# Performance work log

Measured on AMD Instinct MI355X. Metric: run time of the kernel, lower is better.

## Reference

```python
import jax, jax.numpy as jnp
import numpy as np

H, HD, C = 16, 64, 64            # num_heads, head_dim, mini_batch_size
BASE_LR = 1.0
EPS = 1e-6                        # ttt LN eps (ln_fwd / ln_fused_l2_bwd)


def _l2norm(x):
    return x / jnp.maximum(jnp.linalg.norm(x, axis=-1, keepdims=True), 1e-12)


def _ln_fwd(x, g, b):
    mu = x.mean(-1, keepdims=True)
    var = x.var(-1, keepdims=True)
    return g * ((x - mu) * jax.lax.rsqrt(var + EPS)) + b


def _ln_l2_bwd(x, tgt, g, b):
    # gradient of ||LN(x)*g+b - tgt||^2 / 2 wrt x
    D = x.shape[-1]
    mu = x.mean(-1, keepdims=True)
    var = x.var(-1, keepdims=True)
    std = jnp.sqrt(var + EPS)
    xh = (x - mu) / std
    gout = (g * xh + b) - tgt
    gxh = gout * g
    return (D * gxh - gxh.sum(-1, keepdims=True) - xh * (gxh * xh).sum(-1, keepdims=True)) / (D * std)


def setup_inputs() -> dict:
    key = jax.random.key(0)
    ks = jax.random.split(key, 12)
    B, L, D = 4, 8192, 1024
    std = 0.02
    return {
        'hidden_states': jax.random.normal(ks[0], (B, L, D), jnp.float32),
        'wq_w': jax.random.normal(ks[1], (D, D), jnp.float32) * std,
        'wq_b': jnp.zeros((D,), jnp.float32),
        'wk_w': jax.random.normal(ks[2], (D, D), jnp.float32) * std,
        'wk_b': jnp.zeros((D,), jnp.float32),
        'wv_w': jax.random.normal(ks[3], (D, D), jnp.float32) * std,
        'wv_b': jnp.zeros((D,), jnp.float32),
        'wo_w': jax.random.normal(ks[4], (D, D), jnp.float32) * std,
        'wo_b': jnp.zeros((D,), jnp.float32),
        'ttt_norm_weight': jnp.ones((H, HD), jnp.float32),
        'ttt_norm_bias': jnp.zeros((H, HD), jnp.float32),
        'ttt_lr_weight': jax.random.normal(ks[5], (H, 1, D), jnp.float32) * std,
        'ttt_lr_bias': jnp.zeros((H, 1), jnp.float32),
        'W1': jax.random.normal(ks[6], (H, HD, HD), jnp.float32) * std,
        'b1': jnp.zeros((H, 1, HD), jnp.float32),
        'post_norm_w': jnp.ones((D,), jnp.float32),
        'post_norm_b': jnp.zeros((D,), jnp.float32),
    }


def _forward(hidden_states, wq_w, wq_b, wk_w, wk_b, wv_w, wv_b, wo_w, wo_b,
             ttt_norm_weight, ttt_norm_bias, ttt_lr_weight, ttt_lr_bias,
             W1, b1, post_norm_w, post_norm_b):
    B, L, D = hidden_states.shape
    NC = L // C
    XQ = (hidden_states @ wq_w.T + wq_b).reshape(B, L, H, HD)
    XK = (hidden_states @ wk_w.T + wk_b).reshape(B, L, H, HD)
    XV = (hidden_states @ wv_w.T + wv_b).reshape(B, L, H, HD)
    XQ = _l2norm(XQ)
    XK = _l2norm(XK)
    # ln_reconstruction_target (uses sample std, ddof=1, eps=1e-5 on std)
    d = XV - XK
    mu = d.mean(-1, keepdims=True)
    sd = d.std(-1, keepdims=True, ddof=1)
    XV = ttt_norm_weight[None, None] * ((d - mu) / (sd + 1e-5)) + ttt_norm_bias[None, None] + XK
    # reshape to mini-batches: [B,H,NC,C,HD]
    Xmb = hidden_states.reshape(B, NC, C, D)
    to_mb = lambda t: t.transpose(0, 2, 1, 3).reshape(B, H, NC, C, HD)
    XQ, XK, XV = to_mb(XQ), to_mb(XK), to_mb(XV)
    # eta: sigmoid lr gate per token, row-broadcast over mini-batch
    ttt_lr = jax.nn.sigmoid(jnp.einsum('bnkc,hdc->bhnkd', Xmb, ttt_lr_weight)
                            + ttt_lr_bias.reshape(1, H, 1, 1, 1))     # [B,H,NC,C,1]
    eta = jnp.swapaxes(ttt_lr, -1, -2) * (BASE_LR / HD / C)           # [B,H,NC,1,C]
    mask = jnp.tril(jnp.ones((C, C), hidden_states.dtype))
    g = ttt_norm_weight[None, :, None, :]
    bta = ttt_norm_bias[None, :, None, :]
    W0 = jnp.broadcast_to(W1[None], (B, H, HD, HD))
    b0 = jnp.broadcast_to(b1[None], (B, H, 1, HD))

    def step(carry, xs):
        W, bvec = carry
        xq, xk, xv, eta_row = xs                      # eta_row: [B,H,1,C]
        Z1 = xk @ W + bvec                            # [B,H,C,HD]
        grad = _ln_l2_bwd(Z1, xv - xk, g, bta)        # [B,H,C,HD]
        Attn = mask * jnp.einsum('bhid,bhjd->bhij', xq, xk)   # [B,H,C,C]
        eta_full = jnp.broadcast_to(eta_row, Attn.shape)      # [B,H,C,C]
        b1_bar = bvec - (mask * eta_full) @ grad              # [B,H,C,HD]
        Z1_bar = xq @ W - (eta_full * Attn) @ grad + b1_bar
        last_eta = eta_full[..., -1, :, None]                 # [B,H,C,1]
        W_new = W - jnp.einsum('bhcd,bhce->bhde', last_eta * xk, grad)
        b_new = bvec - (last_eta * grad).sum(-2, keepdims=True)
        out = xq + _ln_fwd(Z1_bar, g, bta)
        return (W_new, b_new), out

    xs = (jnp.moveaxis(XQ, 2, 0), jnp.moveaxis(XK, 2, 0),
          jnp.moveaxis(XV, 2, 0), jnp.moveaxis(eta, 2, 0))
    _, outs = jax.lax.scan(step, (W0, b0), xs)        # outs: [NC,B,H,C,HD]
    y = jnp.moveaxis(outs, 0, 2).reshape(B, H, L, HD).transpose(0, 2, 1, 3).reshape(B, L, D)
    # post LayerNorm (eps=1e-6) + output projection
    mu2 = y.mean(-1, keepdims=True)
    var2 = y.var(-1, keepdims=True)
    y = post_norm_w * ((y - mu2) * jax.lax.rsqrt(var2 + 1e-6)) + post_norm_b
    return y @ wo_w.T + wo_b


def reference(hidden_states, wq_w, wq_b, wk_w, wk_b, wv_w, wv_b, wo_w, wo_b,
              ttt_norm_weight, ttt_norm_bias, ttt_lr_weight, ttt_lr_bias,
              W1, b1, post_norm_w, post_norm_b):
    return _forward(hidden_states, wq_w, wq_b, wk_w, wk_b, wv_w, wv_b, wo_w, wo_b,
                    ttt_norm_weight, ttt_norm_bias, ttt_lr_weight, ttt_lr_bias,
                    W1, b1, post_norm_w, post_norm_b)
```

## Files before the change

kernel.cpp:

```cpp
#include <hip/hip_runtime.h>


typedef __attribute__((ext_vector_type(8))) short short8;
typedef __attribute__((ext_vector_type(4))) float f32x4;
typedef __attribute__((ext_vector_type(4))) unsigned short us4;

__device__ __forceinline__ float bf2f(unsigned short s) {
  union { unsigned int u; float f; } c;
  c.u = ((unsigned int)s) << 16;
  return c.f;
}
__device__ __forceinline__ unsigned short f2bf(float f) {
  union { float f; unsigned int u; } c;
  c.f = f;
  unsigned int u = c.u;
  return (unsigned short)((u + 0x7FFFu + ((u >> 16) & 1u)) >> 16);
}

__device__ __forceinline__ void gload_lds16(const void* g, void* l) {
  __builtin_amdgcn_global_load_lds(
      (const __attribute__((address_space(1))) unsigned int*)g,
      (__attribute__((address_space(3))) unsigned int*)l, 16, 0, 0);
}

__device__ __forceinline__ float dpp16_sum(float x) {
  int v = __float_as_int(x);
  x += __int_as_float(__builtin_amdgcn_update_dpp(v, v, 0xB1, 0xF, 0xF, true));
  v = __float_as_int(x);
  x += __int_as_float(__builtin_amdgcn_update_dpp(v, v, 0x4E, 0xF, 0xF, true));
  v = __float_as_int(x);
  x += __int_as_float(__builtin_amdgcn_update_dpp(v, v, 0x141, 0xF, 0xF, true));
  v = __float_as_int(x);
  x += __int_as_float(__builtin_amdgcn_update_dpp(v, v, 0x140, 0xF, 0xF, true));
  return x;
}

__device__ __forceinline__ void barrier_fast() {
  __builtin_amdgcn_sched_barrier(0);
  asm volatile("s_waitcnt lgkmcnt(0)" ::: "memory");
  __builtin_amdgcn_s_barrier();
  asm volatile("" ::: "memory");
  __builtin_amdgcn_sched_barrier(0);
}
__device__ __forceinline__ void bar_nowait() {
  __builtin_amdgcn_sched_barrier(0);
  asm volatile("" ::: "memory");
  __builtin_amdgcn_s_barrier();
  asm volatile("" ::: "memory");
  __builtin_amdgcn_sched_barrier(0);
}

__global__ __launch_bounds__(256) void cvt_f32_bf16(
    const float* __restrict__ in, unsigned short* __restrict__ out, long n) {
  long i = ((long)blockIdx.x * 256 + threadIdx.x) * 4;
  if (i + 3 < n) {
    float4 v = *(const float4*)&in[i];
    us4 o = { f2bf(v.x), f2bf(v.y), f2bf(v.z), f2bf(v.w) };
    *(us4*)&out[i] = o;
  }
}

__global__ __launch_bounds__(256) void build_wcat(
    const float* __restrict__ wq, const float* __restrict__ wk,
    const float* __restrict__ wv, const float* __restrict__ lrw,
    const float* __restrict__ wqb, const float* __restrict__ wkb,
    const float* __restrict__ wvb, const float* __restrict__ lrb,
    unsigned short* __restrict__ Wcat, float* __restrict__ biasc) {
  int i = blockIdx.x * 256 + threadIdx.x;
  int row = i >> 10, col = i & 1023;
  float v;
  if (row < 1024)      v = wq[i];
  else if (row < 2048) v = wk[i - 1048576];
  else if (row < 3072) v = wv[i - 2097152];
  else if (row < 3088) v = lrw[(row - 3072) * 1024 + col];
  else                 v = 0.f;
  Wcat[i] = f2bf(v);
  if (i < 3328) {
    float bv;
    if (i < 1024)      bv = wqb[i];
    else if (i < 2048) bv = wkb[i - 1024];
    else if (i < 3072) bv = wvb[i - 2048];
    else if (i < 3088) bv = lrb[i - 3072];
    else               bv = 0.f;
    biasc[i] = bv;
  }
}

template <int WRITE_BF16>
__global__ __launch_bounds__(512, 1) void gemm256(
    const unsigned short* __restrict__ A, const unsigned short* __restrict__ B,
    const float* __restrict__ bias, void* __restrict__ Cout,
    long M, long N, long K, int NTILN, long ldc) {
  __shared__ __align__(16) unsigned short g_lds[65536];
  char* ldsc = (char*)g_lds;
  const int tid = threadIdx.x, lane = tid & 63, wid = tid >> 6;
  const int wm = wid >> 2, wn = wid & 3;
  const int l15 = lane & 15, lg = lane >> 4;

  unsigned nwg = gridDim.x, bid = blockIdx.x;
  unsigned cpx = nwg >> 3;
  unsigned swz = (bid & 7) * cpx + (bid >> 3);
  unsigned nidx = swz % (unsigned)NTILN, midx = swz / (unsigned)NTILN;
  const long m0 = (long)midx * 256, n0 = (long)nidx * 256;
  const long ldab = K * 2;

  const int srow = wid * 16 + (lane >> 2);
  const int scol = ((lane & 3) * 16) ^ (((lane >> 3) & 3) << 4);
  const int sdst = wid * 1024;
  const char* Ab = (const char*)A;
  const char* Bb = (const char*)B;

  const int acol = (lg * 16) ^ (((l15 >> 1) & 3) << 4);
  const int aro = (wm * 128 + l15) * 64 + acol;
  const int bro = 65536 + (wn * 64 + l15) * 64 + acol;

#define STG_A(tt, h, bb)                                                     \
  gload_lds16(Ab + (size_t)(m0 + (h) * 128 + srow) * ldab + (size_t)(tt) * 64 \
                  + scol,                                                     \
              ldsc + (bb) * 16384 + (h) * 8192 + sdst)
#define STG_B(tt, h, bb)                                                     \
  gload_lds16(Bb + (size_t)(n0 + (h) * 128 + srow) * ldab + (size_t)(tt) * 64 \
                  + scol,                                                     \
              ldsc + 65536 + (bb) * 16384 + (h) * 8192 + sdst)

  f32x4 acc[8][4];
#pragma unroll
  for (int m = 0; m < 8; ++m)
#pragma unroll
    for (int n = 0; n < 4; ++n) acc[m][n] = (f32x4){0.f, 0.f, 0.f, 0.f};

  const int NT = (int)(K >> 5);

#pragma unroll
  for (int tt = 0; tt < 3; ++tt) {
    STG_A(tt, 0, tt); STG_A(tt, 1, tt);
    STG_B(tt, 0, tt); STG_B(tt, 1, tt);
  }
  asm volatile("s_waitcnt vmcnt(8)" ::: "memory");
  bar_nowait();

#pragma unroll 1
  for (int t = 0; t < NT; ++t) {
    const int buf = t & 3, sb = (t + 3) & 3;
    const bool doStage = (t + 3 < NT);
    const char* ab = ldsc + buf * 16384 + aro;
    const char* bb = ldsc + buf * 16384 + bro;

    short8 av[4], bv[4];
#pragma unroll
    for (int i = 0; i < 4; ++i) av[i] = *(const short8*)(ab + i * 1024);
#pragma unroll
    for (int nf = 0; nf < 4; ++nf) bv[nf] = *(const short8*)(bb + nf * 1024);
    if (doStage) { STG_A(t + 3, 0, sb); STG_A(t + 3, 1, sb); }
    bar_nowait();
    __builtin_amdgcn_s_setprio(1);
#pragma unroll
    for (int i = 0; i < 4; ++i)
#pragma unroll
      for (int nf = 0; nf < 4; ++nf)
        acc[i][nf] = __builtin_amdgcn_mfma_f32_16x16x32_bf16(av[i], bv[nf],
                                                             acc[i][nf], 0, 0, 0);
    __builtin_amdgcn_s_setprio(0);
    bar_nowait();

#pragma unroll
    for (int i = 0; i < 4; ++i) av[i] = *(const short8*)(ab + 4096 + i * 1024);
    if (doStage) { STG_B(t + 3, 0, sb); STG_B(t + 3, 1, sb); }
    bar_nowait();
    __builtin_amdgcn_s_setprio(1);
#pragma unroll
    for (int i = 0; i < 4; ++i)
#pragma unroll
      for (int nf = 0; nf < 4; ++nf)
        acc[4 + i][nf] = __builtin_amdgcn_mfma_f32_16x16x32_bf16(
            av[i], bv[nf], acc[4 + i][nf], 0, 0, 0);
    __builtin_amdgcn_s_setprio(0);
    asm volatile("s_waitcnt vmcnt(8)" ::: "memory");
    bar_nowait();
  }
#undef STG_A
#undef STG_B

#pragma unroll
  for (int mf = 0; mf < 8; ++mf) {
    long r0 = m0 + wm * 128 + mf * 16 + lg * 4;
#pragma unroll
    for (int nf = 0; nf < 4; ++nf) {
      long c = n0 + wn * 64 + nf * 16 + l15;
      float bvv = bias ? bias[c] : 0.f;
#pragma unroll
      for (int j = 0; j < 4; ++j) {
        float v = acc[mf][nf][j] + bvv;
        if (WRITE_BF16)
          ((unsigned short*)Cout)[(r0 + j) * ldc + c] = f2bf(v);
        else
          ((float*)Cout)[(r0 + j) * ldc + c] = v;
      }
    }
  }
}

__global__ __launch_bounds__(256) void stage2(
    const unsigned short* __restrict__ QKVL, const float* __restrict__ tnw,
    const float* __restrict__ tnb, unsigned short* __restrict__ XQn,
    unsigned short* __restrict__ XKn, unsigned short* __restrict__ TGT,
    float* __restrict__ eta_buf) {
  int wid = threadIdx.x >> 6, lane = threadIdx.x & 63;
  long idx = (long)blockIdx.x * 4 + wid;
  long t = idx >> 4;
  int h = (int)(idx & 15);
  size_t base = (size_t)t * 3328;
  float q = bf2f(QKVL[base + h * 64 + lane]);
  float k = bf2f(QKVL[base + 1024 + h * 64 + lane]);
  float v = bf2f(QKVL[base + 2048 + h * 64 + lane]);
  float sq = q * q, sk = k * k;
#pragma unroll
  for (int o = 1; o < 64; o <<= 1) {
    sq += __shfl_xor(sq, o);
    sk += __shfl_xor(sk, o);
  }
  float qn = q / fmaxf(sqrtf(sq), 1e-12f);
  float kn = k / fmaxf(sqrtf(sk), 1e-12f);
  float d = v - kn;
  float s1 = d, s2 = d * d;
#pragma unroll
  for (int o = 1; o < 64; o <<= 1) {
    s1 += __shfl_xor(s1, o);
    s2 += __shfl_xor(s2, o);
  }
  float mu = s1 * 0.015625f;
  float var1 = fmaxf(s2 - 64.f * mu * mu, 0.f) * (1.f / 63.f);
  float sd = sqrtf(var1);
  float tgt = tnw[h * 64 + lane] * ((d - mu) / (sd + 1e-5f)) + tnb[h * 64 + lane];
  size_t ob = (size_t)t * 1024 + h * 64 + lane;
  XQn[ob] = f2bf(qn);
  XKn[ob] = f2bf(kn);
  TGT[ob] = f2bf(tgt);
  if (lane == 0) {
    float logit = bf2f(QKVL[base + 3072 + h]);
    float sig = 1.f / (1.f + expf(-logit));
    long bb = t >> 13, l = t & 8191;
    eta_buf[(size_t)(bb * 16 + h) * 8192 + l] = sig * (1.f / 4096.f);
  }
}

__global__ __launch_bounds__(512, 1) void ttt_scan(
    const unsigned short* __restrict__ XQ, const unsigned short* __restrict__ XK,
    const unsigned short* __restrict__ TG, const float* __restrict__ eta_buf,
    const float* __restrict__ W1, const float* __restrict__ b1,
    const float* __restrict__ tnw, const float* __restrict__ tnb,
    float* __restrict__ y) {
  const int bh = blockIdx.x;
  const int b = bh >> 4, h = bh & 15;
  const int tid = threadIdx.x;
  const int lane = tid & 63, wid = tid >> 6;
  const bool isA = wid < 4;
  const int q = wid & 3;
  const int l15 = lane & 15, lg = lane >> 4;

  __shared__ __align__(16) unsigned short xq_s[2][64 * 72];
  __shared__ __align__(16) unsigned short tg_s[2][64 * 72];
  __shared__ __align__(16) unsigned short xk_s[2][64 * 72];
  __shared__ __align__(16) unsigned short gc_s[64 * 72];
  __shared__ __align__(16) unsigned short gradT[64 * 72];
  __shared__ __align__(16) unsigned short xkTe[64 * 72];
  __shared__ __align__(16) unsigned short WT_b[2][64 * 72];
  __shared__ float eta_s[2][64];
  __shared__ float bpart[4][64];

  const size_t tokb = (size_t)b * 8192;
  const int col0 = h * 64;
  const int rr_ = q * 16 + (lane >> 3);
  const int c8_ = (lane & 7) * 8;

  short8 pA0[2], pA1[2], pB0[2];
  float peta = 0.f;
  float bstv[4], gwv[4], gbv[4];
  f32x4 Wreg[4];

  if (isA) {
#pragma unroll
    for (int n = 0; n < 4; ++n) {
      int e = n * 16 + l15;
      bstv[n] = b1[h * 64 + e];
      gwv[n] = tnw[h * 64 + e];
      gbv[n] = tnb[h * 64 + e];
    }
#pragma unroll
    for (int j = 0; j < 2; ++j) {
      size_t g = (tokb + rr_ + j * 8) * 1024 + col0 + c8_;
      pA0[j] = *(const short8*)&XQ[g];
      pA1[j] = *(const short8*)&TG[g];
    }
#pragma unroll
    for (int j = 0; j < 2; ++j) {
      int rr = rr_ + j * 8;
      *(short8*)&xq_s[0][rr * 72 + c8_] = pA0[j];
      *(short8*)&tg_s[0][rr * 72 + c8_] = pA1[j];
    }
#pragma unroll
    for (int j = 0; j < 2; ++j) {
      size_t g = (tokb + 64 + rr_ + j * 8) * 1024 + col0 + c8_;
      pA0[j] = *(const short8*)&XQ[g];
      pA1[j] = *(const short8*)&TG[g];
    }
  } else {
#pragma unroll
    for (int j = 0; j < 2; ++j)
      pB0[j] = *(const short8*)&XK[(tokb + rr_ + j * 8) * 1024 + col0 + c8_];
#pragma unroll
    for (int j = 0; j < 2; ++j)
      *(short8*)&xk_s[0][(rr_ + j * 8) * 72 + c8_] = pB0[j];
#pragma unroll
    for (int j = 0; j < 2; ++j)
      pB0[j] = *(const short8*)&XK[(tokb + 64 + rr_ + j * 8) * 1024 + col0 + c8_];
#pragma unroll
    for (int n = 0; n < 4; ++n)
#pragma unroll
      for (int jj = 0; jj < 4; ++jj) {
        int d = q * 16 + lg * 4 + jj, e = n * 16 + l15;
        float w = W1[h * 4096 + d * 64 + e];
        Wreg[n][jj] = w;
        WT_b[0][e * 72 + d] = f2bf(w);
      }
    if (wid == 4) {
      eta_s[0][lane] = eta_buf[(size_t)bh * 8192 + lane];
      peta = eta_buf[(size_t)bh * 8192 + 64 + lane];
    }
  }
  __syncthreads();

  for (int nc = 0; nc < 128; ++nc) {
    const int p = nc & 1;
    const unsigned short* WTc = WT_b[p];
    unsigned short* WTn = WT_b[p ^ 1];

    if (isA) {
      if (nc) {
#pragma unroll
        for (int n = 0; n < 4; ++n) {
          int e = n * 16 + l15;
          bstv[n] -= bpart[0][e] + bpart[1][e] + bpart[2][e] + bpart[3][e];
        }
      }
      if (nc + 1 < 128) {
#pragma unroll
        for (int j = 0; j < 2; ++j) {
          int rr = rr_ + j * 8;
          *(short8*)&xq_s[p ^ 1][rr * 72 + c8_] = pA0[j];
          *(short8*)&tg_s[p ^ 1][rr * 72 + c8_] = pA1[j];
        }
      }
      if (nc + 2 < 128) {
#pragma unroll
        for (int j = 0; j < 2; ++j) {
          size_t g = (tokb + (nc + 2) * 64 + rr_ + j * 8) * 1024 + col0 + c8_;
          pA0[j] = *(const short8*)&XQ[g];
          pA1[j] = *(const short8*)&TG[g];
        }
      }
      f32x4 accZ[4];
#pragma unroll
      for (int n = 0; n < 4; ++n)
        accZ[n] = (f32x4){bstv[n], bstv[n], bstv[n], bstv[n]};
      __builtin_amdgcn_s_setprio(1);
#pragma unroll
      for (int kk = 0; kk < 2; ++kk) {
        const int ko = kk * 32 + lg * 8;
        short8 a_xk = *(const short8*)&xk_s[p][(q * 16 + l15) * 72 + ko];
#pragma unroll
        for (int n = 0; n < 4; ++n) {
          short8 b_w = *(const short8*)&WTc[(n * 16 + l15) * 72 + ko];
          accZ[n] = __builtin_amdgcn_mfma_f32_16x16x32_bf16(a_xk, b_w, accZ[n], 0, 0, 0);
        }
      }
      __builtin_amdgcn_s_setprio(0);
      float grv[4][4];
#pragma unroll
      for (int j = 0; j < 4; ++j) {
        const int r = q * 16 + lg * 4 + j;
        float z[4], s1 = 0.f, s2 = 0.f;
#pragma unroll
        for (int n = 0; n < 4; ++n) {
          z[n] = accZ[n][j];
          s1 += z[n];
          s2 += z[n] * z[n];
        }
        s1 = dpp16_sum(s1);
        s2 = dpp16_sum(s2);
        float mu = s1 * 0.015625f;
        float var = s2 * 0.015625f - mu * mu;
        float rstd = rsqrtf(var + 1e-6f);
        float xh[4], gx[4], s3 = 0.f, s4 = 0.f;
#pragma unroll
        for (int n = 0; n < 4; ++n) {
          xh[n] = (z[n] - mu) * rstd;
          float tg = bf2f(tg_s[p][r * 72 + n * 16 + l15]);
          float go = gwv[n] * xh[n] + gbv[n] - tg;
          gx[n] = go * gwv[n];
          s3 += gx[n];
          s4 += gx[n] * xh[n];
        }
        s3 = dpp16_sum(s3);
        s4 = dpp16_sum(s4);
#pragma unroll
        for (int n = 0; n < 4; ++n)
          grv[n][j] = (64.f * gx[n] - s3 - xh[n] * s4) * rstd * 0.015625f;
      }
#pragma unroll
      for (int n = 0; n < 4; ++n) {
        us4 pk = {f2bf(grv[n][0]), f2bf(grv[n][1]), f2bf(grv[n][2]),
                  f2bf(grv[n][3])};
        *(us4*)&gradT[(n * 16 + l15) * 72 + q * 16 + lg * 4] = pk;
      }
    } else {
      if (nc + 1 < 128) {
#pragma unroll
        for (int j = 0; j < 2; ++j)
          *(short8*)&xk_s[p ^ 1][(rr_ + j * 8) * 72 + c8_] = pB0[j];
        if (wid == 4) eta_s[p ^ 1][lane] = peta;
      }
      if (nc + 2 < 128) {
#pragma unroll
        for (int j = 0; j < 2; ++j)
          pB0[j] = *(const short8*)
              &XK[(tokb + (nc + 2) * 64 + rr_ + j * 8) * 1024 + col0 + c8_];
        if (wid == 4) peta = eta_buf[(size_t)bh * 8192 + (nc + 2) * 64 + lane];
      }
#pragma unroll
      for (int it = 0; it < 4; ++it) {
        int c0 = q * 16 + it * 4;
        us4 pk;
#pragma unroll
        for (int u = 0; u < 4; ++u)
          pk[u] = f2bf(-eta_s[p][c0 + u] * bf2f(xk_s[p][(c0 + u) * 72 + lane]));
        *(us4*)&xkTe[lane * 72 + c0] = pk;
      }
      f32x4 accA[4];
#pragma unroll
      for (int n = 0; n < 4; ++n) accA[n] = (f32x4){0.f, 0.f, 0.f, 0.f};
      __builtin_amdgcn_s_setprio(1);
#pragma unroll
      for (int kk = 0; kk < 2; ++kk) {
        const int ko = kk * 32 + lg * 8;
        short8 a_xq = *(const short8*)&xq_s[p][(q * 16 + l15) * 72 + ko];
#pragma unroll
        for (int n = 0; n < 4; ++n) {
          short8 b_k = *(const short8*)&xk_s[p][(n * 16 + l15) * 72 + ko];
          accA[n] = __builtin_amdgcn_mfma_f32_16x16x32_bf16(a_xq, b_k, accA[n], 0, 0, 0);
        }
      }
      __builtin_amdgcn_s_setprio(0);
#pragma unroll
      for (int j = 0; j < 4; ++j) {
        const int r = q * 16 + lg * 4 + j;
#pragma unroll
        for (int n = 0; n < 4; ++n) {
          int cj = n * 16 + l15;
          float v = (cj <= r) ? (-eta_s[p][cj] * (1.f + accA[n][j])) : 0.f;
          gc_s[r * 72 + cj] = f2bf(v);
        }
      }
    }
    barrier_fast();

    if (isA) {
      f32x4 accZb[4];
#pragma unroll
      for (int n = 0; n < 4; ++n)
        accZb[n] = (f32x4){bstv[n], bstv[n], bstv[n], bstv[n]};
      __builtin_amdgcn_s_setprio(1);
#pragma unroll
      for (int kk = 0; kk < 2; ++kk) {
        const int ko = kk * 32 + lg * 8;
        short8 a_xq = *(const short8*)&xq_s[p][(q * 16 + l15) * 72 + ko];
        short8 a_gc = *(const short8*)&gc_s[(q * 16 + l15) * 72 + ko];
#pragma unroll
        for (int n = 0; n < 4; ++n) {
          short8 b_w = *(const short8*)&WTc[(n * 16 + l15) * 72 + ko];
          short8 b_g = *(const short8*)&gradT[(n * 16 + l15) * 72 + ko];
          accZb[n] = __builtin_amdgcn_mfma_f32_16x16x32_bf16(a_xq, b_w, accZb[n], 0, 0, 0);
          accZb[n] = __builtin_amdgcn_mfma_f32_16x16x32_bf16(a_gc, b_g, accZb[n], 0, 0, 0);
        }
      }
      __builtin_amdgcn_s_setprio(0);
#pragma unroll
      for (int j = 0; j < 4; ++j) {
        const int r = q * 16 + lg * 4 + j;
        float z[4], s1 = 0.f, s2 = 0.f;
#pragma unroll
        for (int n = 0; n < 4; ++n) {
          z[n] = accZb[n][j];
          s1 += z[n];
          s2 += z[n] * z[n];
        }
        s1 = dpp16_sum(s1);
        s2 = dpp16_sum(s2);
        float mu = s1 * 0.015625f;
        float var = s2 * 0.015625f - mu * mu;
        float rstd = rsqrtf(var + 1e-6f);
        size_t gbase = (tokb + nc * 64 + r) * 1024 + col0;
#pragma unroll
        for (int n = 0; n < 4; ++n) {
          int e = n * 16 + l15;
          float ov = bf2f(xq_s[p][r * 72 + e]) + gwv[n] * ((z[n] - mu) * rstd) + gbv[n];
          y[gbase + e] = ov;
        }
      }
    } else {
      f32x4 accW[4];
#pragma unroll
      for (int n = 0; n < 4; ++n) accW[n] = Wreg[n];
      __builtin_amdgcn_s_setprio(1);
#pragma unroll
      for (int kk = 0; kk < 2; ++kk) {
        const int ko = kk * 32 + lg * 8;
        short8 a_ke = *(const short8*)&xkTe[(q * 16 + l15) * 72 + ko];
#pragma unroll
        for (int n = 0; n < 4; ++n) {
          short8 b_g = *(const short8*)&gradT[(n * 16 + l15) * 72 + ko];
          accW[n] = __builtin_amdgcn_mfma_f32_16x16x32_bf16(a_ke, b_g, accW[n], 0, 0, 0);
        }
      }
      __builtin_amdgcn_s_setprio(0);
#pragma unroll
      for (int n = 0; n < 4; ++n) {
        Wreg[n] = accW[n];
        us4 pk = {f2bf(accW[n][0]), f2bf(accW[n][1]), f2bf(accW[n][2]),
                  f2bf(accW[n][3])};
        *(us4*)&WTn[(n * 16 + l15) * 72 + q * 16 + lg * 4] = pk;
      }
      {
        float s = 0.f;
#pragma unroll
        for (int it = 0; it < 4; ++it) {
          us4 gv = *(const us4*)&gradT[lane * 72 + q * 16 + it * 4];
#pragma unroll
          for (int u = 0; u < 4; ++u)
            s += eta_s[p][q * 16 + it * 4 + u] * bf2f(gv[u]);
        }
        bpart[q][lane] = s;
      }
    }
    barrier_fast();
  }
}

__global__ __launch_bounds__(256) void postnorm(
    const float* __restrict__ yv, const float* __restrict__ pw,
    const float* __restrict__ pb, unsigned short* __restrict__ yn) {
  int t = blockIdx.x;
  int tid = threadIdx.x, lane = tid & 63, wid = tid >> 6;
  const float* row = yv + (size_t)t * 1024;
  float4 v = *(const float4*)&row[tid * 4];
  float s1 = v.x + v.y + v.z + v.w;
  float s2 = v.x * v.x + v.y * v.y + v.z * v.z + v.w * v.w;
#pragma unroll
  for (int o = 1; o < 64; o <<= 1) {
    s1 += __shfl_xor(s1, o);
    s2 += __shfl_xor(s2, o);
  }
  __shared__ float r1[4], r2[4];
  if (lane == 0) {
    r1[wid] = s1;
    r2[wid] = s2;
  }
  __syncthreads();
  s1 = r1[0] + r1[1] + r1[2] + r1[3];
  s2 = r2[0] + r2[1] + r2[2] + r2[3];
  float mu = s1 * (1.f / 1024.f);
  float var = s2 * (1.f / 1024.f) - mu * mu;
  float rstd = rsqrtf(var + 1e-6f);
  int c = tid * 4;
  us4 o4 = {f2bf(pw[c] * ((v.x - mu) * rstd) + pb[c]),
            f2bf(pw[c + 1] * ((v.y - mu) * rstd) + pb[c + 1]),
            f2bf(pw[c + 2] * ((v.z - mu) * rstd) + pb[c + 2]),
            f2bf(pw[c + 3] * ((v.w - mu) * rstd) + pb[c + 3])};
  *(us4*)&yn[(size_t)t * 1024 + c] = o4;
}

extern "C" void kernel_launch(void* const* d_in, const int* in_sizes, int n_in,
                              void* d_out, int out_size, void* d_ws,
                              size_t ws_size, hipStream_t stream) {
  const float* hs  = (const float*)d_in[0];
  const float* wqw = (const float*)d_in[1];
  const float* wqb = (const float*)d_in[2];
  const float* wkw = (const float*)d_in[3];
  const float* wkb = (const float*)d_in[4];
  const float* wvw = (const float*)d_in[5];
  const float* wvb = (const float*)d_in[6];
  const float* wow = (const float*)d_in[7];
  const float* wob = (const float*)d_in[8];
  const float* tnw = (const float*)d_in[9];
  const float* tnb = (const float*)d_in[10];
  const float* lrw = (const float*)d_in[11];
  const float* lrb = (const float*)d_in[12];
  const float* W1  = (const float*)d_in[13];
  const float* b1  = (const float*)d_in[14];
  const float* pnw = (const float*)d_in[15];
  const float* pnb = (const float*)d_in[16];

  const size_t OFF_WCAT  = 67108864;
  const size_t OFF_BIASC = OFF_WCAT + 6815744;
  const size_t OFF_WOBF  = OFF_BIASC + 16384;
  const size_t OFF_QKVL  = OFF_WOBF + 2097152;
  const size_t OFF_XK    = OFF_QKVL + 218103808;
  const size_t OFF_TGT   = OFF_XK + 67108864;
  const size_t OFF_ETA   = OFF_TGT + 67108864;
  const size_t NEEDED    = OFF_ETA + 2097152;
  if (ws_size < NEEDED) return;

  char* ws = (char*)d_ws;
  unsigned short* hs_bf = (unsigned short*)ws;
  unsigned short* XQn   = (unsigned short*)ws;
  unsigned short* Wcat  = (unsigned short*)(ws + OFF_WCAT);
  float* biasc          = (float*)(ws + OFF_BIASC);
  unsigned short* wo_bf = (unsigned short*)(ws + OFF_WOBF);
  unsigned short* QKVL  = (unsigned short*)(ws + OFF_QKVL);
  float* yv             = (float*)(ws + OFF_QKVL);
  unsigned short* ynorm = (unsigned short*)(ws + OFF_QKVL + 134217728);
  unsigned short* XKn   = (unsigned short*)(ws + OFF_XK);
  unsigned short* TGT   = (unsigned short*)(ws + OFF_TGT);
  float* eta_buf        = (float*)(ws + OFF_ETA);

  cvt_f32_bf16<<<32768, 256, 0, stream>>>(hs, hs_bf, 33554432L);
  build_wcat<<<13312, 256, 0, stream>>>(wqw, wkw, wvw, lrw, wqb, wkb, wvb, lrb,
                                        Wcat, biasc);
  cvt_f32_bf16<<<1024, 256, 0, stream>>>(wow, wo_bf, 1048576L);
  gemm256<1><<<1664, 512, 0, stream>>>(hs_bf, Wcat, biasc, QKVL,
                                       32768L, 3328L, 1024L, 13, 3328L);
  stage2<<<131072, 256, 0, stream>>>(QKVL, tnw, tnb, XQn, XKn, TGT, eta_buf);
  ttt_scan<<<64, 512, 0, stream>>>(XQn, XKn, TGT, eta_buf, W1, b1, tnw, tnb, yv);
  postnorm<<<32768, 256, 0, stream>>>(yv, pnw, pnb, ynorm);
  gemm256<0><<<512, 512, 0, stream>>>(ynorm, wo_bf, wob, d_out,
                                      32768L, 1024L, 1024L, 4, 1024L);
}
```

Baseline: 956.2 us.

## Fuse QKV projection with L2-norm, target LN and eta into GEMM epilogue

Reorders the concatenated QKV weight so each 256-column GEMM tile holds one head's q, k, v and lr-logit columns. The per-head L2 normalisation, reconstruction-target LayerNorm and sigmoid eta are then computed in the GEMM epilogue, and the separate stage2 kernel is removed. This avoids writing and re-reading the large bf16 QKVL intermediate, at the cost of padding N from 3328 to 4096, which adds GEMM work. It also hoists the LDS loads ahead of the MFMAs in the W update of the scan kernel and reshuffles the workspace layout.

```diff
diff --git a/kernel.cpp b/kernel.cpp
--- a/kernel.cpp
+++ b/kernel.cpp
@@ -68,21 +68,211 @@
     unsigned short* __restrict__ Wcat, float* __restrict__ biasc) {
   int i = blockIdx.x * 256 + threadIdx.x;
   int row = i >> 10, col = i & 1023;
+  int h = row >> 8, o = row & 255;
   float v;
-  if (row < 1024)      v = wq[i];
-  else if (row < 2048) v = wk[i - 1048576];
-  else if (row < 3072) v = wv[i - 2097152];
-  else if (row < 3088) v = lrw[(row - 3072) * 1024 + col];
-  else                 v = 0.f;
+  if (o < 64)        v = wq[(h * 64 + o) * 1024 + col];
+  else if (o < 128)  v = wk[(h * 64 + o - 64) * 1024 + col];
+  else if (o < 192)  v = wv[(h * 64 + o - 128) * 1024 + col];
+  else if (o == 192) v = lrw[h * 1024 + col];
+  else               v = 0.f;
   Wcat[i] = f2bf(v);
-  if (i < 3328) {
+  if (i < 4096) {
+    int hh = i >> 8, oo = i & 255;
     float bv;
-    if (i < 1024)      bv = wqb[i];
-    else if (i < 2048) bv = wkb[i - 1024];
-    else if (i < 3072) bv = wvb[i - 2048];
-    else if (i < 3088) bv = lrb[i - 3072];
-    else               bv = 0.f;
+    if (oo < 64)        bv = wqb[hh * 64 + oo];
+    else if (oo < 128)  bv = wkb[hh * 64 + oo - 64];
+    else if (oo < 192)  bv = wvb[hh * 64 + oo - 128];
+    else if (oo == 192) bv = lrb[hh];
+    else                bv = 0.f;
     biasc[i] = bv;
+  }
+}
+
+__global__ __launch_bounds__(512, 1) void gemm256_qkv(
+    const unsigned short* __restrict__ A, const unsigned short* __restrict__ B,
+    const float* __restrict__ bias, const float* __restrict__ tnw,
+    const float* __restrict__ tnb, unsigned short* __restrict__ XQn,
+    unsigned short* __restrict__ XKn, unsigned short* __restrict__ TGT,
+    float* __restrict__ eta, long M, long K) {
+  __shared__ __align__(16) unsigned short g_lds[65536];
+  char* ldsc = (char*)g_lds;
+  const int tid = threadIdx.x, lane = tid & 63, wid = tid >> 6;
+  const int wm = wid >> 2, wn = wid & 3;
+  const int l15 = lane & 15, lg = lane >> 4;
+  const int NTILN = 16;
+
+  unsigned nwg = gridDim.x, bid = blockIdx.x;
+  unsigned cpx = nwg >> 3;
+  unsigned swz = (bid & 7) * cpx + (bid >> 3);
+  unsigned nidx = swz % (unsigned)NTILN, midx = swz / (unsigned)NTILN;
+  const long m0 = (long)midx * 256, n0 = (long)nidx * 256;
+  const long ldab = K * 2;
+
+  const int srow = wid * 16 + (lane >> 2);
+  const int scol = ((lane & 3) * 16) ^ (((lane >> 3) & 3) << 4);
+  const int sdst = wid * 1024;
+  const char* Ab = (const char*)A;
+  const char* Bb = (const char*)B;
+
+  const int acol = (lg * 16) ^ (((l15 >> 1) & 3) << 4);
+  const int aro = (wm * 128 + l15) * 64 + acol;
+  const int bro = 65536 + (wn * 64 + l15) * 64 + acol;
+
+#define STG_A(tt, h, bb)                                                      \
+  gload_lds16(Ab + (size_t)(m0 + (h) * 128 + srow) * ldab + (size_t)(tt) * 64 \
+                  + scol,                                                     \
+              ldsc + (bb) * 16384 + (h) * 8192 + sdst)
+#define STG_B(tt, h, bb)                                                      \
+  gload_lds16(Bb + (size_t)(n0 + (h) * 128 + srow) * ldab + (size_t)(tt) * 64 \
+                  + scol,                                                     \
+              ldsc + 65536 + (bb) * 16384 + (h) * 8192 + sdst)
+
+  f32x4 acc[8][4];
+#pragma unroll
+  for (int m = 0; m < 8; ++m)
+#pragma unroll
+    for (int n = 0; n < 4; ++n) acc[m][n] = (f32x4){0.f, 0.f, 0.f, 0.f};
+
+  const int NT = (int)(K >> 5);
+
+#pragma unroll
+  for (int tt = 0; tt < 3; ++tt) {
+    STG_A(tt, 0, tt); STG_A(tt, 1, tt);
+    STG_B(tt, 0, tt); STG_B(tt, 1, tt);
+  }
+  asm volatile("s_waitcnt vmcnt(8)" ::: "memory");
+  bar_nowait();
+
+#pragma unroll 1
+  for (int t = 0; t < NT; ++t) {
+    const int buf = t & 3, sb = (t + 3) & 3;
+    const bool doStage = (t + 3 < NT);
+    const char* ab = ldsc + buf * 16384 + aro;
+    const char* bb = ldsc + buf * 16384 + bro;
+
+    short8 av[4], bv[4];
+#pragma unroll
+    for (int i = 0; i < 4; ++i) av[i] = *(const short8*)(ab + i * 1024);
+#pragma unroll
+    for (int nf = 0; nf < 4; ++nf) bv[nf] = *(const short8*)(bb + nf * 1024);
+    if (doStage) { STG_A(t + 3, 0, sb); STG_A(t + 3, 1, sb); }
+    bar_nowait();
+    __builtin_amdgcn_s_setprio(1);
+#pragma unroll
+    for (int i = 0; i < 4; ++i)
+#pragma unroll
+      for (int nf = 0; nf < 4; ++nf)
+        acc[i][nf] = __builtin_amdgcn_mfma_f32_16x16x32_bf16(av[i], bv[nf],
+                                                             acc[i][nf], 0, 0, 0);
+    __builtin_amdgcn_s_setprio(0);
+    bar_nowait();
+
+#pragma unroll
+    for (int i = 0; i < 4; ++i) av[i] = *(const short8*)(ab + 4096 + i * 1024);
+    if (doStage) { STG_B(t + 3, 0, sb); STG_B(t + 3, 1, sb); }
+    bar_nowait();
+    __builtin_amdgcn_s_setprio(1);
+#pragma unroll
+    for (int i = 0; i < 4; ++i)
+#pragma unroll
+      for (int nf = 0; nf < 4; ++nf)
+        acc[4 + i][nf] = __builtin_amdgcn_mfma_f32_16x16x32_bf16(
+            av[i], bv[nf], acc[4 + i][nf], 0, 0, 0);
+    __builtin_amdgcn_s_setprio(0);
+    asm volatile("s_waitcnt vmcnt(8)" ::: "memory");
+    bar_nowait();
+  }
+#undef STG_A
+#undef STG_B
+
+  const int h = (int)nidx;
+  float bcol[4], twv[4], tbv[4];
+#pragma unroll
+  for (int nf = 0; nf < 4; ++nf) {
+    bcol[nf] = bias[n0 + wn * 64 + nf * 16 + l15];
+    twv[nf] = tnw[h * 64 + nf * 16 + l15];
+    tbv[nf] = tnb[h * 64 + nf * 16 + l15];
+  }
+  __syncthreads();
+  unsigned short* kn_s = g_lds;
+
+  if (wn == 0) {
+#pragma unroll
+    for (int mf = 0; mf < 8; ++mf)
+#pragma unroll
+      for (int j = 0; j < 4; ++j) {
+        float v[4], s2 = 0.f;
+#pragma unroll
+        for (int nf = 0; nf < 4; ++nf) {
+          v[nf] = acc[mf][nf][j] + bcol[nf];
+          s2 += v[nf] * v[nf];
+        }
+        s2 = dpp16_sum(s2);
+        float rn = 1.f / fmaxf(sqrtf(s2), 1e-12f);
+        size_t tt = (size_t)(m0 + wm * 128 + mf * 16 + lg * 4 + j);
+#pragma unroll
+        for (int nf = 0; nf < 4; ++nf)
+          XQn[tt * 1024 + h * 64 + nf * 16 + l15] = f2bf(v[nf] * rn);
+      }
+  } else if (wn == 1) {
+#pragma unroll
+    for (int mf = 0; mf < 8; ++mf)
+#pragma unroll
+      for (int j = 0; j < 4; ++j) {
+        float v[4], s2 = 0.f;
+#pragma unroll
+        for (int nf = 0; nf < 4; ++nf) {
+          v[nf] = acc[mf][nf][j] + bcol[nf];
+          s2 += v[nf] * v[nf];
+        }
+        s2 = dpp16_sum(s2);
+        float rn = 1.f / fmaxf(sqrtf(s2), 1e-12f);
+        size_t tt = (size_t)(m0 + wm * 128 + mf * 16 + lg * 4 + j);
+        int lr_ = wm * 128 + mf * 16 + lg * 4 + j;
+#pragma unroll
+        for (int nf = 0; nf < 4; ++nf) {
+          unsigned short kb = f2bf(v[nf] * rn);
+          XKn[tt * 1024 + h * 64 + nf * 16 + l15] = kb;
+          kn_s[lr_ * 72 + nf * 16 + l15] = kb;
+        }
+      }
+  }
+  __syncthreads();
+  if (wn == 2) {
+#pragma unroll
+    for (int mf = 0; mf < 8; ++mf)
+#pragma unroll
+      for (int j = 0; j < 4; ++j) {
+        int lr_ = wm * 128 + mf * 16 + lg * 4 + j;
+        float dv[4], s1 = 0.f, s2 = 0.f;
+#pragma unroll
+        for (int nf = 0; nf < 4; ++nf) {
+          float kn = bf2f(kn_s[lr_ * 72 + nf * 16 + l15]);
+          dv[nf] = acc[mf][nf][j] + bcol[nf] - kn;
+          s1 += dv[nf];
+          s2 += dv[nf] * dv[nf];
+        }
+        s1 = dpp16_sum(s1);
+        s2 = dpp16_sum(s2);
+        float mu = s1 * 0.015625f;
+        float var1 = fmaxf(s2 - 64.f * mu * mu, 0.f) * (1.f / 63.f);
+        float rs = 1.f / (sqrtf(var1) + 1e-5f);
+        size_t tt = (size_t)(m0 + wm * 128 + mf * 16 + lg * 4 + j);
+#pragma unroll
+        for (int nf = 0; nf < 4; ++nf)
+          TGT[tt * 1024 + h * 64 + nf * 16 + l15] =
+              f2bf(twv[nf] * ((dv[nf] - mu) * rs) + tbv[nf]);
+      }
+  } else if (wn == 3 && l15 == 0) {
+#pragma unroll
+    for (int mf = 0; mf < 8; ++mf)
+#pragma unroll
+      for (int j = 0; j < 4; ++j) {
+        size_t tt = (size_t)(m0 + wm * 128 + mf * 16 + lg * 4 + j);
+        float lgt = acc[mf][0][j] + bcol[0];
+        float sig = 1.f / (1.f + expf(-lgt));
+        eta[((tt >> 13) * 16 + h) * 8192 + (tt & 8191)] = sig * (1.f / 4096.f);
+      }
   }
 }
 
@@ -114,11 +304,11 @@
   const int aro = (wm * 128 + l15) * 64 + acol;
   const int bro = 65536 + (wn * 64 + l15) * 64 + acol;
 
-#define STG_A(tt, h, bb)                                                     \
+#define STG_A(tt, h, bb)                                                      \
   gload_lds16(Ab + (size_t)(m0 + (h) * 128 + srow) * ldab + (size_t)(tt) * 64 \
                   + scol,                                                     \
               ldsc + (bb) * 16384 + (h) * 8192 + sdst)
-#define STG_B(tt, h, bb)                                                     \
+#define STG_B(tt, h, bb)                                                      \
   gload_lds16(Bb + (size_t)(n0 + (h) * 128 + srow) * ldab + (size_t)(tt) * 64 \
                   + scol,                                                     \
               ldsc + 65536 + (bb) * 16384 + (h) * 8192 + sdst)
@@ -197,50 +387,6 @@
           ((float*)Cout)[(r0 + j) * ldc + c] = v;
       }
     }
-  }
-}
-
-__global__ __launch_bounds__(256) void stage2(
-    const unsigned short* __restrict__ QKVL, const float* __restrict__ tnw,
-    const float* __restrict__ tnb, unsigned short* __restrict__ XQn,
-    unsigned short* __restrict__ XKn, unsigned short* __restrict__ TGT,
-    float* __restrict__ eta_buf) {
-  int wid = threadIdx.x >> 6, lane = threadIdx.x & 63;
-  long idx = (long)blockIdx.x * 4 + wid;
-  long t = idx >> 4;
-  int h = (int)(idx & 15);
-  size_t base = (size_t)t * 3328;
-  float q = bf2f(QKVL[base + h * 64 + lane]);
-  float k = bf2f(QKVL[base + 1024 + h * 64 + lane]);
-  float v = bf2f(QKVL[base + 2048 + h * 64 + lane]);
-  float sq = q * q, sk = k * k;
-#pragma unroll
-  for (int o = 1; o < 64; o <<= 1) {
-    sq += __shfl_xor(sq, o);
-    sk += __shfl_xor(sk, o);
-  }
-  float qn = q / fmaxf(sqrtf(sq), 1e-12f);
-  float kn = k / fmaxf(sqrtf(sk), 1e-12f);
-  float d = v - kn;
-  float s1 = d, s2 = d * d;
-#pragma unroll
-  for (int o = 1; o < 64; o <<= 1) {
-    s1 += __shfl_xor(s1, o);
-    s2 += __shfl_xor(s2, o);
-  }
-  float mu = s1 * 0.015625f;
-  float var1 = fmaxf(s2 - 64.f * mu * mu, 0.f) * (1.f / 63.f);
-  float sd = sqrtf(var1);
-  float tgt = tnw[h * 64 + lane] * ((d - mu) / (sd + 1e-5f)) + tnb[h * 64 + lane];
-  size_t ob = (size_t)t * 1024 + h * 64 + lane;
-  XQn[ob] = f2bf(qn);
-  XKn[ob] = f2bf(kn);
-  TGT[ob] = f2bf(tgt);
-  if (lane == 0) {
-    float logit = bf2f(QKVL[base + 3072 + h]);
-    float sig = 1.f / (1.f + expf(-logit));
-    long bb = t >> 13, l = t & 8191;
-    eta_buf[(size_t)(bb * 16 + h) * 8192 + l] = sig * (1.f / 4096.f);
   }
 }
 
@@ -508,20 +654,25 @@
         }
       }
     } else {
+      short8 a_ke[2], b_g[2][4];
+#pragma unroll
+      for (int kk = 0; kk < 2; ++kk) {
+        const int ko = kk * 32 + lg * 8;
+        a_ke[kk] = *(const short8*)&xkTe[(q * 16 + l15) * 72 + ko];
+#pragma unroll
+        for (int n = 0; n < 4; ++n)
+          b_g[kk][n] = *(const short8*)&gradT[(n * 16 + l15) * 72 + ko];
+      }
       f32x4 accW[4];
 #pragma unroll
       for (int n = 0; n < 4; ++n) accW[n] = Wreg[n];
       __builtin_amdgcn_s_setprio(1);
 #pragma unroll
-      for (int kk = 0; kk < 2; ++kk) {
-        const int ko = kk * 32 + lg * 8;
-        short8 a_ke = *(const short8*)&xkTe[(q * 16 + l15) * 72 + ko];
-#pragma unroll
-        for (int n = 0; n < 4; ++n) {
-          short8 b_g = *(const short8*)&gradT[(n * 16 + l15) * 72 + ko];
-          accW[n] = __builtin_amdgcn_mfma_f32_16x16x32_bf16(a_ke, b_g, accW[n], 0, 0, 0);
-        }
-      }
+      for (int kk = 0; kk < 2; ++kk)
+#pragma unroll
+        for (int n = 0; n < 4; ++n)
+          accW[n] = __builtin_amdgcn_mfma_f32_16x16x32_bf16(a_ke[kk], b_g[kk][n],
+                                                            accW[n], 0, 0, 0);
       __builtin_amdgcn_s_setprio(0);
 #pragma unroll
       for (int n = 0; n < 4; ++n) {
@@ -600,36 +751,38 @@
   const float* pnw = (const float*)d_in[15];
   const float* pnb = (const float*)d_in[16];
 
-  const size_t OFF_WCAT  = 67108864;
-  const size_t OFF_BIASC = OFF_WCAT + 6815744;
-  const size_t OFF_WOBF  = OFF_BIASC + 16384;
-  const size_t OFF_QKVL  = OFF_WOBF + 2097152;
-  const size_t OFF_XK    = OFF_QKVL + 218103808;
-  const size_t OFF_TGT   = OFF_XK + 67108864;
-  const size_t OFF_ETA   = OFF_TGT + 67108864;
-  const size_t NEEDED    = OFF_ETA + 2097152;
+  const size_t OFF_XQ    = 0;
+  const size_t OFF_XK    = 67108864;
+  const size_t OFF_TGT   = 134217728;
+  const size_t OFF_ETA   = 201326592;
+  const size_t OFF_WOBF  = OFF_ETA + 2097152;
+  const size_t OFF_HSBF  = OFF_WOBF + 2097152;
+  const size_t OFF_WCAT  = OFF_HSBF + 67108864;
+  const size_t OFF_BIASC = OFF_WCAT + 8388608;
+  const size_t OFF_YV    = OFF_HSBF;
+  const size_t NEEDED_A  = OFF_BIASC + 16384;
+  const size_t NEEDED_B  = OFF_YV + 134217728;
+  const size_t NEEDED    = NEEDED_A > NEEDED_B ? NEEDED_A : NEEDED_B;
   if (ws_size < NEEDED) return;
 
   char* ws = (char*)d_ws;
-  unsigned short* hs_bf = (unsigned short*)ws;
-  unsigned short* XQn   = (unsigned short*)ws;
-  unsigned short* Wcat  = (unsigned short*)(ws + OFF_WCAT);
-  float* biasc          = (float*)(ws + OFF_BIASC);
-  unsigned short* wo_bf = (unsigned short*)(ws + OFF_WOBF);
-  unsigned short* QKVL  = (unsigned short*)(ws + OFF_QKVL);
-  float* yv             = (float*)(ws + OFF_QKVL);
-  unsigned short* ynorm = (unsigned short*)(ws + OFF_QKVL + 134217728);
+  unsigned short* XQn   = (unsigned short*)(ws + OFF_XQ);
+  unsigned short* ynorm = (unsigned short*)(ws + OFF_XQ);
   unsigned short* XKn   = (unsigned short*)(ws + OFF_XK);
   unsigned short* TGT   = (unsigned short*)(ws + OFF_TGT);
   float* eta_buf        = (float*)(ws + OFF_ETA);
+  unsigned short* wo_bf = (unsigned short*)(ws + OFF_WOBF);
+  unsigned short* hs_bf = (unsigned short*)(ws + OFF_HSBF);
+  unsigned short* Wcat  = (unsigned short*)(ws + OFF_WCAT);
+  float* biasc          = (float*)(ws + OFF_BIASC);
+  float* yv             = (float*)(ws + OFF_YV);
 
   cvt_f32_bf16<<<32768, 256, 0, stream>>>(hs, hs_bf, 33554432L);
-  build_wcat<<<13312, 256, 0, stream>>>(wqw, wkw, wvw, lrw, wqb, wkb, wvb, lrb,
+  build_wcat<<<16384, 256, 0, stream>>>(wqw, wkw, wvw, lrw, wqb, wkb, wvb, lrb,
                                         Wcat, biasc);
   cvt_f32_bf16<<<1024, 256, 0, stream>>>(wow, wo_bf, 1048576L);
-  gemm256<1><<<1664, 512, 0, stream>>>(hs_bf, Wcat, biasc, QKVL,
-                                       32768L, 3328L, 1024L, 13, 3328L);
-  stage2<<<131072, 256, 0, stream>>>(QKVL, tnw, tnb, XQn, XKn, TGT, eta_buf);
+  gemm256_qkv<<<2048, 512, 0, stream>>>(hs_bf, Wcat, biasc, tnw, tnb,
+                                        XQn, XKn, TGT, eta_buf, 32768L, 1024L);
   ttt_scan<<<64, 512, 0, stream>>>(XQn, XKn, TGT, eta_buf, W1, b1, tnw, tnb, yv);
   postnorm<<<32768, 256, 0, stream>>>(yv, pnw, pnb, ynorm);
   gemm256<0><<<512, 512, 0, stream>>>(ynorm, wo_bf, wob, d_out,
```

New measurement: 889.4 us. -7.0%, faster.
